# Performance work log

Measured on AMD Instinct MI355X. Metric: run time of the kernel, lower is better.

## Reference

```python
import jax, jax.numpy as jnp
import numpy as np

DIM = 1024
NUM_HEADS = 16
HEAD_DIM = DIM // NUM_HEADS
MLP_HIDDEN = 4 * DIM
SCALE = HEAD_DIM ** -0.5
EPS = 1e-5


def setup_inputs() -> dict:
    key = jax.random.key(0)
    ks = jax.random.split(key, 6)
    s = (2.0 / DIM) ** 0.5
    sd = (2.0 / MLP_HIDDEN) ** 0.5
    return {
        "x": jax.random.normal(ks[0], (2, 2048, DIM), dtype=jnp.float32),
        "attn_qkv_weight": jax.random.normal(ks[1], (3 * DIM, DIM), dtype=jnp.float32) * s,
        "attn_out_weight": jax.random.normal(ks[2], (DIM, DIM), dtype=jnp.float32) * s,
        "norm1_weight": jnp.ones((DIM,), jnp.float32),
        "norm1_bias": jnp.zeros((DIM,), jnp.float32),
        "mlp_gate_weight": jax.random.normal(ks[3], (MLP_HIDDEN, DIM), dtype=jnp.float32) * s,
        "mlp_up_weight": jax.random.normal(ks[4], (MLP_HIDDEN, DIM), dtype=jnp.float32) * s,
        "mlp_down_weight": jax.random.normal(ks[5], (DIM, MLP_HIDDEN), dtype=jnp.float32) * sd,
        "norm2_weight": jnp.ones((DIM,), jnp.float32),
        "norm2_bias": jnp.zeros((DIM,), jnp.float32),
    }


def _layer_norm(x, w, b):
    mean = x.mean(axis=-1, keepdims=True)
    var = jnp.mean(jnp.square(x - mean), axis=-1, keepdims=True)
    return (x - mean) / jnp.sqrt(var + EPS) * w + b


def reference(x, attn_qkv_weight, attn_out_weight, norm1_weight, norm1_bias,
              mlp_gate_weight, mlp_up_weight, mlp_down_weight, norm2_weight, norm2_bias):
    B, S, D = x.shape
    residual1 = x
    xn = _layer_norm(x, norm1_weight, norm1_bias)
    qkv = xn @ attn_qkv_weight.T                      # [B,S,3D]
    qkv = qkv.reshape(B, S, 3, NUM_HEADS, HEAD_DIM).transpose(2, 0, 3, 1, 4)
    q, k, v = qkv[0], qkv[1], qkv[2]                  # [B,H,S,hd]
    scores = jnp.einsum('bhqd,bhkd->bhqk', q, k) * SCALE  # full O(S^2) matrix
    attn = jax.nn.softmax(scores, axis=-1)            # no causal mask (default False)
    out = jnp.einsum('bhqk,bhkd->bhqd', attn, v)      # [B,H,S,hd]
    out = out.transpose(0, 2, 1, 3).reshape(B, S, D)
    x2 = residual1 + out @ attn_out_weight.T
    xn2 = _layer_norm(x2, norm2_weight, norm2_bias)
    gate = xn2 @ mlp_gate_weight.T
    up = xn2 @ mlp_up_weight.T
    hidden = jax.nn.silu(gate) * up
    return x2 + hidden @ mlp_down_weight.T
```

## Files before the change

### kernel.cpp

```cpp
#include <hip/hip_runtime.h>

typedef float f32x4 __attribute__((ext_vector_type(4)));
typedef __bf16 bf16x8 __attribute__((ext_vector_type(8)));
typedef unsigned int u32;

#define DEV __device__ __forceinline__
#define WAITVM(n) asm volatile("s_waitcnt vmcnt(" #n ")" ::: "memory")

DEV void gload_lds16(const void* g, void* l) {
  __builtin_amdgcn_global_load_lds(
      (const __attribute__((address_space(1))) u32*)g,
      (__attribute__((address_space(3))) u32*)l, 16, 0, 0);
}

DEV int xcd_swz(int flat, int nwg) {
  return (flat & 7) * (nwg >> 3) + (flat >> 3);
}

__global__ __launch_bounds__(256) void cvt_bf16(const float* __restrict__ in,
                                                __bf16* __restrict__ o, int n) {
  int i = (blockIdx.x * 256 + threadIdx.x) * 8;
  if (i >= n) return;
  float4 a = *(const float4*)(in + i);
  float4 b = *(const float4*)(in + i + 4);
  union { bf16x8 v; __bf16 e[8]; } u;
  u.e[0] = (__bf16)a.x; u.e[1] = (__bf16)a.y; u.e[2] = (__bf16)a.z; u.e[3] = (__bf16)a.w;
  u.e[4] = (__bf16)b.x; u.e[5] = (__bf16)b.y; u.e[6] = (__bf16)b.z; u.e[7] = (__bf16)b.w;
  *(bf16x8*)(o + i) = u.v;
}

__global__ __launch_bounds__(256) void ln_kernel(const float* __restrict__ x,
                                                 const float* __restrict__ w,
                                                 const float* __restrict__ b,
                                                 __bf16* __restrict__ o) {
  const int row = blockIdx.x, tid = threadIdx.x;
  const float4 v = ((const float4*)(x + (size_t)row * 1024))[tid];
  float s  = v.x + v.y + v.z + v.w;
  float s2 = v.x * v.x + v.y * v.y + v.z * v.z + v.w * v.w;
  for (int off = 32; off; off >>= 1) {
    s  += __shfl_down(s, off);
    s2 += __shfl_down(s2, off);
  }
  __shared__ float rs[4], rs2[4];
  if ((tid & 63) == 0) { rs[tid >> 6] = s; rs2[tid >> 6] = s2; }
  __syncthreads();
  float S = rs[0] + rs[1] + rs[2] + rs[3];
  float S2 = rs2[0] + rs2[1] + rs2[2] + rs2[3];
  float mean = S * (1.0f / 1024.0f);
  float var = S2 * (1.0f / 1024.0f) - mean * mean;
  float inv = rsqrtf(var + 1e-5f);
  const float4 wv = ((const float4*)w)[tid];
  const float4 bv = ((const float4*)b)[tid];
  union { ushort4 u4; __bf16 e[4]; } u;
  u.e[0] = (__bf16)((v.x - mean) * inv * wv.x + bv.x);
  u.e[1] = (__bf16)((v.y - mean) * inv * wv.y + bv.y);
  u.e[2] = (__bf16)((v.z - mean) * inv * wv.z + bv.z);
  u.e[3] = (__bf16)((v.w - mean) * inv * wv.w + bv.w);
  *(ushort4*)(o + (size_t)row * 1024 + tid * 4) = u.u4;
}


template <int EPI, int MI>
__global__ __launch_bounds__(256) void gemm_bt(const __bf16* __restrict__ A,
                                               const __bf16* __restrict__ B,
                                               void* __restrict__ Cout,
                                               const float* __restrict__ Res,
                                               int M, int N, int K) {
  constexpr int BM = MI * 32;
  __shared__ __align__(16) __bf16 As[3][BM * 32];
  __shared__ __align__(16) __bf16 Bs[3][128 * 32];
  const int tid = threadIdx.x;
  const int lane = tid & 63;
  const int w = tid >> 6;
  const int wr = w >> 1, wc = w & 1;
  const int l15 = lane & 15, g = lane >> 4;
  const int c8 = ((g + (l15 >> 1)) & 3) * 8;

  const int nbx = gridDim.x;
  const int logical = xcd_swz(blockIdx.y * nbx + blockIdx.x, nbx * gridDim.y);
  const int bm = (logical / nbx) * BM, bn = (logical % nbx) * 128;

  f32x4 acc[MI][4] = {};

  auto stage = [&](int buf, int k0) {
#pragma unroll
    for (int p = 0; p < MI / 2; ++p) {
      const int ch = p * 256 + tid;
      const int row = ch >> 2;
      const int gc = ((ch & 3) - ((ch >> 3) & 3)) & 3;
      gload_lds16(A + (size_t)(bm + row) * K + k0 + gc * 8,
                  &As[buf][(p * 256 + w * 64) * 8]);
    }
#pragma unroll
    for (int p = 0; p < 2; ++p) {
      const int ch = p * 256 + tid;
      const int row = ch >> 2;
      const int gc = ((ch & 3) - ((ch >> 3) & 3)) & 3;
      gload_lds16(B + (size_t)(bn + row) * K + k0 + gc * 8,
                  &Bs[buf][(p * 256 + w * 64) * 8]);
    }
  };

  const int NT = K >> 5;
  stage(0, 0);
  stage(1, 32);

  int cur = 0;
  for (int t = 0; t < NT; ++t) {
    if (t + 1 < NT) {
      if constexpr (MI == 4) { WAITVM(4); } else { WAITVM(3); }
    } else {
      WAITVM(0);
    }
    __builtin_amdgcn_s_barrier();
    if (t + 2 < NT) {
      int sb = cur + 2; if (sb >= 3) sb -= 3;
      stage(sb, (t + 2) * 32);
    }
    bf16x8 af[MI], bfr[4];
#pragma unroll
    for (int i = 0; i < MI; ++i)
      af[i] = *(const bf16x8*)(&As[cur][(wr * (MI * 16) + i * 16 + l15) * 32 + c8]);
#pragma unroll
    for (int j = 0; j < 4; ++j)
      bfr[j] = *(const bf16x8*)(&Bs[cur][(wc * 64 + j * 16 + l15) * 32 + c8]);
#pragma unroll
    for (int i = 0; i < MI; ++i)
#pragma unroll
      for (int j = 0; j < 4; ++j)
        acc[i][j] = __builtin_amdgcn_mfma_f32_16x16x32_bf16(af[i], bfr[j], acc[i][j], 0, 0, 0);
    cur = (cur == 2) ? 0 : cur + 1;
  }

  const int r0 = bm + wr * (MI * 16) + g * 4;
  const int c0 = bn + wc * 64 + l15;
#pragma unroll
  for (int i = 0; i < MI; ++i)
#pragma unroll
    for (int j = 0; j < 4; ++j)
#pragma unroll
      for (int r = 0; r < 4; ++r) {
        const size_t idx = (size_t)(r0 + i * 16 + r) * N + (c0 + j * 16);
        const float v = acc[i][j][r];
        if (EPI == 0) ((__bf16*)Cout)[idx] = (__bf16)v;
        else          ((float*)Cout)[idx] = v + Res[idx];
      }
}

__global__ __launch_bounds__(256, 2) void gemm_mlp(const __bf16* __restrict__ A,
                                                   const __bf16* __restrict__ BG,
                                                   const __bf16* __restrict__ BU,
                                                   __bf16* __restrict__ H,
                                                   int M, int N, int K) {
  __shared__ __align__(16) __bf16 As[3][128 * 32];
  __shared__ __align__(16) __bf16 Bg[3][128 * 32];
  __shared__ __align__(16) __bf16 Bu[3][128 * 32];
  const int tid = threadIdx.x;
  const int lane = tid & 63;
  const int w = tid >> 6;
  const int wr = w >> 1, wc = w & 1;
  const int l15 = lane & 15, g = lane >> 4;
  const int c8 = ((g + (l15 >> 1)) & 3) * 8;

  const int nbx = gridDim.x;
  const int logical = xcd_swz(blockIdx.y * nbx + blockIdx.x, nbx * gridDim.y);
  const int bm = (logical / nbx) * 128, bn = (logical % nbx) * 128;

  f32x4 accg[4][4] = {};
  f32x4 accu[4][4] = {};

  auto stage = [&](int buf, int k0) {
#pragma unroll
    for (int p = 0; p < 2; ++p) {
      const int ch = p * 256 + tid;
      const int row = ch >> 2;
      const int gc = ((ch & 3) - ((ch >> 3) & 3)) & 3;
      const int coff = gc * 8;
      const int dst = (p * 256 + w * 64) * 8;
      gload_lds16(A + (size_t)(bm + row) * K + k0 + coff, &As[buf][dst]);
      gload_lds16(BG + (size_t)(bn + row) * K + k0 + coff, &Bg[buf][dst]);
      gload_lds16(BU + (size_t)(bn + row) * K + k0 + coff, &Bu[buf][dst]);
    }
  };

  const int NT = K >> 5;
  stage(0, 0);
  stage(1, 32);

  int cur = 0;
  for (int t = 0; t < NT; ++t) {
    if (t + 1 < NT) { WAITVM(6); } else { WAITVM(0); }
    __builtin_amdgcn_s_barrier();
    if (t + 2 < NT) {
      int sb = cur + 2; if (sb >= 3) sb -= 3;
      stage(sb, (t + 2) * 32);
    }
    bf16x8 af[4], bgf[4], buf_[4];
#pragma unroll
    for (int i = 0; i < 4; ++i)
      af[i] = *(const bf16x8*)(&As[cur][(wr * 64 + i * 16 + l15) * 32 + c8]);
#pragma unroll
    for (int j = 0; j < 4; ++j) {
      bgf[j] = *(const bf16x8*)(&Bg[cur][(wc * 64 + j * 16 + l15) * 32 + c8]);
      buf_[j] = *(const bf16x8*)(&Bu[cur][(wc * 64 + j * 16 + l15) * 32 + c8]);
    }
#pragma unroll
    for (int i = 0; i < 4; ++i)
#pragma unroll
      for (int j = 0; j < 4; ++j) {
        accg[i][j] = __builtin_amdgcn_mfma_f32_16x16x32_bf16(af[i], bgf[j], accg[i][j], 0, 0, 0);
        accu[i][j] = __builtin_amdgcn_mfma_f32_16x16x32_bf16(af[i], buf_[j], accu[i][j], 0, 0, 0);
      }
    cur = (cur == 2) ? 0 : cur + 1;
  }

  const int r0 = bm + wr * 64 + g * 4;
  const int c0 = bn + wc * 64 + l15;
#pragma unroll
  for (int i = 0; i < 4; ++i)
#pragma unroll
    for (int j = 0; j < 4; ++j)
#pragma unroll
      for (int r = 0; r < 4; ++r) {
        const float gt = accg[i][j][r];
        const float ut = accu[i][j][r];
        const float h = gt / (1.0f + __expf(-gt)) * ut;
        H[(size_t)(r0 + i * 16 + r) * N + (c0 + j * 16)] = (__bf16)h;
      }
}

__global__ __launch_bounds__(256) void transpose_v(const __bf16* __restrict__ qkv,
                                                   __bf16* __restrict__ vT) {
  const int st = blockIdx.x, bh = blockIdx.y;
  const int b = bh >> 4, h = bh & 15;
  __shared__ __bf16 tile[64][80];
  const int tid = threadIdx.x;
#pragma unroll
  for (int it = 0; it < 2; ++it) {
    const int idx = it * 256 + tid;
    const int r = idx >> 3, c0 = (idx & 7) * 8;
    bf16x8 v = *(const bf16x8*)(qkv + (size_t)(b * 2048 + st * 64 + r) * 3072 + 2048 + h * 64 + c0);
    *(bf16x8*)&tile[r][c0] = v;
  }
  __syncthreads();
#pragma unroll
  for (int it = 0; it < 2; ++it) {
    const int idx = it * 256 + tid;
    const int d = idx >> 3, s0 = (idx & 7) * 8;
    union { bf16x8 v; __bf16 e[8]; } u;
#pragma unroll
    for (int j = 0; j < 8; ++j) u.e[j] = tile[s0 + j][d];
    *(bf16x8*)(vT + (size_t)(bh * 64 + d) * 2048 + st * 64 + s0) = u.v;
  }
}

__global__ __launch_bounds__(256) void attn_kernel(const __bf16* __restrict__ qkv,
                                                   const __bf16* __restrict__ vT,
                                                   __bf16* __restrict__ outp) {
  const int logical = xcd_swz(blockIdx.y * 32 + blockIdx.x, 1024);
  const int qt = logical & 31, bh = logical >> 5;
  const int b = bh >> 4, h = bh & 15;
  const int tid = threadIdx.x, lane = tid & 63, w = tid >> 6;
  const int l15 = lane & 15, g = lane >> 4;
  const float CSC = 0.125f * 1.44269504f;

  __shared__ __align__(16) __bf16 Ks[64 * 64];
  __shared__ __align__(16) __bf16 Vs[64 * 64];
  __shared__ __align__(16) __bf16 Ps[4][16 * 80];

  const int qrow = qt * 64 + w * 16 + l15;
  const size_t qbase = (size_t)(b * 2048 + qrow) * 3072 + h * 64;
  const bf16x8 qf0 = *(const bf16x8*)(qkv + qbase + g * 8);
  const bf16x8 qf1 = *(const bf16x8*)(qkv + qbase + 32 + g * 8);

  f32x4 o_acc[4] = {};
  float l_r[4] = {0.f, 0.f, 0.f, 0.f};

  const size_t kgbase = (size_t)(b * 2048) * 3072 + 1024 + h * 64;
  const size_t vgbase = (size_t)bh * 64 * 2048;

  for (int t = 0; t < 32; ++t) {
    const int kv0 = t * 64;
#pragma unroll
    for (int p = 0; p < 2; ++p) {
      const int ch = p * 256 + w * 64 + lane;
      const int row = ch >> 3, c = ch & 7;
      const int gc = c ^ (row & 7);
      gload_lds16(qkv + kgbase + (size_t)(kv0 + row) * 3072 + gc * 8, Ks + (p * 256 + w * 64) * 8);
      gload_lds16(vT + vgbase + (size_t)row * 2048 + kv0 + gc * 8, Vs + (p * 256 + w * 64) * 8);
    }
    WAITVM(0);
    __syncthreads();

    f32x4 sf[4];
    __builtin_amdgcn_s_setprio(1);
#pragma unroll
    for (int ni = 0; ni < 4; ++ni) {
      const int krow = ni * 16 + l15;
      const __bf16* kb = Ks + krow * 64;
      const bf16x8 kf0 = *(const bf16x8*)(kb + ((g ^ (krow & 7)) * 8));
      const bf16x8 kf1 = *(const bf16x8*)(kb + (((4 + g) ^ (krow & 7)) * 8));
      f32x4 z = {0.f, 0.f, 0.f, 0.f};
      z = __builtin_amdgcn_mfma_f32_16x16x32_bf16(qf0, kf0, z, 0, 0, 0);
      z = __builtin_amdgcn_mfma_f32_16x16x32_bf16(qf1, kf1, z, 0, 0, 0);
      sf[ni] = z;
    }
    __builtin_amdgcn_s_setprio(0);

#pragma unroll
    for (int ni = 0; ni < 4; ++ni)
#pragma unroll
      for (int r = 0; r < 4; ++r) {
        const float pv = exp2f(sf[ni][r] * CSC);
        sf[ni][r] = pv;
        l_r[r] += pv;
      }

    __bf16* pw = Ps[w];
#pragma unroll
    for (int ni = 0; ni < 4; ++ni)
#pragma unroll
      for (int r = 0; r < 4; ++r) {
        const int row = g * 4 + r;
        const int pc = (ni * 2 + (l15 >> 3)) ^ (row & 7);
        pw[row * 80 + pc * 8 + (l15 & 7)] = (__bf16)sf[ni][r];
      }
    asm volatile("" ::: "memory");
    const bf16x8 pa0 = *(const bf16x8*)(pw + l15 * 80 + ((g ^ (l15 & 7)) * 8));
    const bf16x8 pa1 = *(const bf16x8*)(pw + l15 * 80 + (((4 + g) ^ (l15 & 7)) * 8));

    __builtin_amdgcn_s_setprio(1);
#pragma unroll
    for (int ni = 0; ni < 4; ++ni) {
      const int vrow = ni * 16 + l15;
      const __bf16* vb = Vs + vrow * 64;
      const bf16x8 vf0 = *(const bf16x8*)(vb + ((g ^ (vrow & 7)) * 8));
      const bf16x8 vf1 = *(const bf16x8*)(vb + (((4 + g) ^ (vrow & 7)) * 8));
      o_acc[ni] = __builtin_amdgcn_mfma_f32_16x16x32_bf16(pa0, vf0, o_acc[ni], 0, 0, 0);
      o_acc[ni] = __builtin_amdgcn_mfma_f32_16x16x32_bf16(pa1, vf1, o_acc[ni], 0, 0, 0);
    }
    __builtin_amdgcn_s_setprio(0);
    __syncthreads();
  }

#pragma unroll
  for (int mk = 1; mk < 16; mk <<= 1)
#pragma unroll
    for (int r = 0; r < 4; ++r) l_r[r] += __shfl_xor(l_r[r], mk);
#pragma unroll
  for (int r = 0; r < 4; ++r) {
    const int orow = qt * 64 + w * 16 + g * 4 + r;
    const float invl = 1.0f / l_r[r];
#pragma unroll
    for (int ni = 0; ni < 4; ++ni)
      outp[(size_t)(b * 2048 + orow) * 1024 + h * 64 + ni * 16 + l15] =
          (__bf16)(o_acc[ni][r] * invl);
  }
}

extern "C" void kernel_launch(void* const* d_in, const int* in_sizes, int n_in,
                              void* d_out, int out_size, void* d_ws, size_t ws_size,
                              hipStream_t stream) {
  const float* x     = (const float*)d_in[0];
  const float* Wqkv  = (const float*)d_in[1];
  const float* Wout  = (const float*)d_in[2];
  const float* n1w   = (const float*)d_in[3];
  const float* n1b   = (const float*)d_in[4];
  const float* Wgate = (const float*)d_in[5];
  const float* Wup   = (const float*)d_in[6];
  const float* Wdown = (const float*)d_in[7];
  const float* n2w   = (const float*)d_in[8];
  const float* n2b   = (const float*)d_in[9];
  float* out = (float*)d_out;
  char* ws = (char*)d_ws;
  const size_t MB = 1u << 20;

  __bf16* XN  = (__bf16*)(ws + 0);
  __bf16* QKV = (__bf16*)(ws + 8 * MB);
  __bf16* VT  = (__bf16*)(ws + 32 * MB);
  __bf16* ATT = (__bf16*)(ws + 40 * MB);
  float*  X2  = (float*)(ws + 48 * MB);
  __bf16* H   = QKV;
  __bf16* WQ  = (__bf16*)(ws + 64 * MB);
  __bf16* WO  = (__bf16*)(ws + 70 * MB);
  __bf16* WG  = (__bf16*)(ws + 72 * MB);
  __bf16* WU  = (__bf16*)(ws + 80 * MB);
  __bf16* WD  = (__bf16*)(ws + 88 * MB);

  cvt_bf16<<<3145728 / 2048, 256, 0, stream>>>(Wqkv, WQ, 3145728);
  cvt_bf16<<<1048576 / 2048, 256, 0, stream>>>(Wout, WO, 1048576);
  cvt_bf16<<<4194304 / 2048, 256, 0, stream>>>(Wgate, WG, 4194304);
  cvt_bf16<<<4194304 / 2048, 256, 0, stream>>>(Wup, WU, 4194304);
  cvt_bf16<<<4194304 / 2048, 256, 0, stream>>>(Wdown, WD, 4194304);

  ln_kernel<<<4096, 256, 0, stream>>>(x, n1w, n1b, XN);
  gemm_bt<0, 4><<<dim3(24, 32), 256, 0, stream>>>(XN, WQ, QKV, nullptr, 4096, 3072, 1024);
  transpose_v<<<dim3(32, 32), 256, 0, stream>>>(QKV, VT);
  attn_kernel<<<dim3(32, 32), 256, 0, stream>>>(QKV, VT, ATT);
  gemm_bt<1, 2><<<dim3(8, 64), 256, 0, stream>>>(ATT, WO, X2, x, 4096, 1024, 1024);
  ln_kernel<<<4096, 256, 0, stream>>>(X2, n2w, n2b, XN);
  gemm_mlp<<<dim3(32, 32), 256, 0, stream>>>(XN, WG, WU, H, 4096, 4096, 1024);
  gemm_bt<1, 2><<<dim3(8, 64), 256, 0, stream>>>(H, WD, out, X2, 4096, 1024, 4096);

  (void)in_sizes; (void)n_in; (void)out_size; (void)ws_size;
}
```

Baseline: 312.0 us.

## Prefetch attention K/V via registers, fold scale into Q, group GEMM tile order

```diff
diff --git a/kernel.cpp b/kernel.cpp
--- a/kernel.cpp
+++ b/kernel.cpp
@@ -78,7 +78,9 @@
 
   const int nbx = gridDim.x;
   const int logical = xcd_swz(blockIdx.y * nbx + blockIdx.x, nbx * gridDim.y);
-  const int bm = (logical / nbx) * BM, bn = (logical % nbx) * 128;
+  const int per = 8 * nbx, grp = logical / per, rem = logical % per;
+  const int bm = (grp * 8 + (rem & 7)) * BM;
+  const int bn = (rem >> 3) * 128;
 
   f32x4 acc[MI][4] = {};
 
@@ -164,7 +166,9 @@
 
   const int nbx = gridDim.x;
   const int logical = xcd_swz(blockIdx.y * nbx + blockIdx.x, nbx * gridDim.y);
-  const int bm = (logical / nbx) * 128, bn = (logical % nbx) * 128;
+  const int per = 8 * nbx, grp = logical / per, rem = logical % per;
+  const int bm = (grp * 8 + (rem & 7)) * 128;
+  const int bn = (rem >> 3) * 128;
 
   f32x4 accg[4][4] = {};
   f32x4 accu[4][4] = {};
@@ -270,8 +274,18 @@
 
   const int qrow = qt * 64 + w * 16 + l15;
   const size_t qbase = (size_t)(b * 2048 + qrow) * 3072 + h * 64;
-  const bf16x8 qf0 = *(const bf16x8*)(qkv + qbase + g * 8);
-  const bf16x8 qf1 = *(const bf16x8*)(qkv + qbase + 32 + g * 8);
+  bf16x8 qf0, qf1;
+  {
+    union { bf16x8 v; __bf16 e[8]; } a, bqq, oa, ob;
+    a.v = *(const bf16x8*)(qkv + qbase + g * 8);
+    bqq.v = *(const bf16x8*)(qkv + qbase + 32 + g * 8);
+#pragma unroll
+    for (int j = 0; j < 8; ++j) {
+      oa.e[j] = (__bf16)((float)a.e[j] * CSC);
+      ob.e[j] = (__bf16)((float)bqq.e[j] * CSC);
+    }
+    qf0 = oa.v; qf1 = ob.v;
+  }
 
   f32x4 o_acc[4] = {};
   float l_r[4] = {0.f, 0.f, 0.f, 0.f};
@@ -279,18 +293,32 @@
   const size_t kgbase = (size_t)(b * 2048) * 3072 + 1024 + h * 64;
   const size_t vgbase = (size_t)bh * 64 * 2048;
 
-  for (int t = 0; t < 32; ++t) {
+  float4 kreg[2], vreg[2];
+  auto issue = [&](int t) {
     const int kv0 = t * 64;
 #pragma unroll
     for (int p = 0; p < 2; ++p) {
       const int ch = p * 256 + w * 64 + lane;
       const int row = ch >> 3, c = ch & 7;
       const int gc = c ^ (row & 7);
-      gload_lds16(qkv + kgbase + (size_t)(kv0 + row) * 3072 + gc * 8, Ks + (p * 256 + w * 64) * 8);
-      gload_lds16(vT + vgbase + (size_t)row * 2048 + kv0 + gc * 8, Vs + (p * 256 + w * 64) * 8);
-    }
-    WAITVM(0);
-    __syncthreads();
+      kreg[p] = *(const float4*)(qkv + kgbase + (size_t)(kv0 + row) * 3072 + gc * 8);
+      vreg[p] = *(const float4*)(vT + vgbase + (size_t)row * 2048 + kv0 + gc * 8);
+    }
+  };
+  auto commit = [&]() {
+#pragma unroll
+    for (int p = 0; p < 2; ++p) {
+      *(float4*)(Ks + (p * 256 + w * 64) * 8 + lane * 8) = kreg[p];
+      *(float4*)(Vs + (p * 256 + w * 64) * 8 + lane * 8) = vreg[p];
+    }
+  };
+
+  issue(0);
+  commit();
+  __syncthreads();
+
+  for (int t = 0; t < 32; ++t) {
+    if (t + 1 < 32) issue(t + 1);
 
     f32x4 sf[4];
     __builtin_amdgcn_s_setprio(1);
@@ -311,7 +339,7 @@
     for (int ni = 0; ni < 4; ++ni)
 #pragma unroll
       for (int r = 0; r < 4; ++r) {
-        const float pv = exp2f(sf[ni][r] * CSC);
+        const float pv = exp2f(sf[ni][r]);
         sf[ni][r] = pv;
         l_r[r] += pv;
       }
@@ -340,7 +368,12 @@
       o_acc[ni] = __builtin_amdgcn_mfma_f32_16x16x32_bf16(pa1, vf1, o_acc[ni], 0, 0, 0);
     }
     __builtin_amdgcn_s_setprio(0);
-    __syncthreads();
+
+    if (t + 1 < 32) {
+      __syncthreads();
+      commit();
+      __syncthreads();
+    }
   }
 
 #pragma unroll
```

Result: slower. 376.7 us (+20.7%).
